# Optimization experiments

Measured on AMD Instinct MI355X. Metric: run time of the kernel, lower is better.

The kernel has to match this reference:

```python
import jax, jax.numpy as jnp
import numpy as np

V, EH, EO, H, O = 32000, 512, 256, 512, 256
S, B = 128, 32
THRESH = 1e-6


def _uniform(key, shape, fan_in):
    bound = 1.0 / np.sqrt(fan_in)
    return jax.random.uniform(key, shape, jnp.float32, -bound, bound)


def setup_inputs() -> dict:
    key = jax.random.key(0)
    ks = jax.random.split(key, 12)
    return {
        "input": jax.random.randint(ks[0], (S, B), 0, V, dtype=jnp.int32),
        # embedding_layer: Linear(V,EH), Linear(EH,EO); stored (in,out)
        "W1": _uniform(ks[1], (V, EH), V),
        "b1": _uniform(ks[2], (EH,), V),
        "W2": _uniform(ks[3], (EH, EO), EH),
        "b2": _uniform(ks[4], (EO,), EH),
        # GRU weights (PyTorch layout: gates stacked r,z,n)
        "W_ih": _uniform(ks[5], (3 * H, EO), H),
        "W_hh": _uniform(ks[6], (3 * H, H), H),
        "b_ih": _uniform(ks[7], (3 * H,), H),
        "b_hh": _uniform(ks[8], (3 * H,), H),
        # head: Linear(H,O)
        "W3": _uniform(ks[9], (H, O), H),
        "b3": _uniform(ks[10], (O,), H),
    }


def reference(input, W1, b1, W2, b2, W_ih, W_hh, b_ih, b_hh, W3, b3):
    thr = lambda x: jnp.where(x > THRESH, x, 0.0)  # nn.Threshold(1e-6, 0)
    # one_hot(input, V) @ W1 == row gather of W1 (same math, no O(V) GEMM)
    emb = thr(thr(W1[input] + b1) @ W2 + b2)  # (S, B, EO)

    # GRU: precompute input projections for all timesteps
    x_proj = emb @ W_ih.T + b_ih  # (S, B, 3H)
    h0 = jnp.zeros((B, H), jnp.float32)

    def step(h, xp):
        gh = h @ W_hh.T + b_hh
        xr, xz, xn = jnp.split(xp, 3, axis=-1)
        hr, hz, hn = jnp.split(gh, 3, axis=-1)
        r = jax.nn.sigmoid(xr + hr)
        z = jax.nn.sigmoid(xz + hz)
        n = jnp.tanh(xn + r * hn)
        h_new = (1.0 - z) * n + z * h
        return h_new, None

    hT, _ = jax.lax.scan(step, h0, x_proj)  # final hidden (B, H)
    # linear head on h_n (dropout in eval mode = identity); torch h_n is (1,B,H)
    out = hT[None, :, :] @ W3 + b3  # (1, B, O)
    return out
```

## Files before the change

### kernel.cpp

```cpp
#include <hip/hip_runtime.h>
#include <cstddef>

#define THRESH 1e-6f
#define SPIN_LIMIT (1 << 20)

__device__ __forceinline__ float thrf(float x) { return x > THRESH ? x : 0.0f; }
__device__ __forceinline__ float sigm(float x) { return 1.0f / (1.0f + expf(-x)); }
__device__ __forceinline__ void fma4(float4& c, float a, float4 b) {
    c.x += a * b.x; c.y += a * b.y; c.z += a * b.z; c.w += a * b.w;
}
__device__ __forceinline__ void macc4(float4& a, float4 w, float4 h) {
    a.x += w.x * h.x; a.y += w.y * h.y; a.z += w.z * h.z; a.w += w.w * h.w;
}
__device__ __forceinline__ float hsum4(float4 a) { return a.x + a.y + a.z + a.w; }

__global__ __launch_bounds__(256) void k_embed_gemm(const int* __restrict__ tok,
                                                    const float* __restrict__ W1,
                                                    const float* __restrict__ b1,
                                                    const float* __restrict__ W2,
                                                    const float* __restrict__ b2,
                                                    float* __restrict__ emb) {
    constexpr int BM = 64, BN = 64, BK = 32, K = 512, N = 256;
    __shared__ float As[BK][BM + 1];
    __shared__ float Bs[BK][BN];

    const int tid = threadIdx.x;
    const int bm = blockIdx.x * BM;
    const int bn = blockIdx.y * BN;
    const int tn = (tid & 15) * 4;
    const int tm = (tid >> 4) * 4;

    float acc[4][4] = {};

    for (int k0 = 0; k0 < K; k0 += BK) {
        for (int i = tid; i < BM * BK / 4; i += 256) {
            int c4 = (i & (BK / 4 - 1)) * 4;
            int r  = i / (BK / 4);
            int tv = tok[bm + r];
            float4 v  = *(const float4*)(W1 + (size_t)tv * K + k0 + c4);
            float4 bb = *(const float4*)(b1 + k0 + c4);
            As[c4 + 0][r] = thrf(v.x + bb.x);
            As[c4 + 1][r] = thrf(v.y + bb.y);
            As[c4 + 2][r] = thrf(v.z + bb.z);
            As[c4 + 3][r] = thrf(v.w + bb.w);
        }
        for (int i = tid; i < BK * BN / 4; i += 256) {
            int n4 = (i & 15) * 4;
            int kk = i >> 4;
            *(float4*)&Bs[kk][n4] = *(const float4*)(W2 + (size_t)(k0 + kk) * N + bn + n4);
        }
        __syncthreads();

        for (int k = 0; k < BK; ++k) {
            float a0 = As[k][tm + 0], a1 = As[k][tm + 1];
            float a2 = As[k][tm + 2], a3 = As[k][tm + 3];
            float b0 = Bs[k][tn + 0], b1v = Bs[k][tn + 1];
            float b2v = Bs[k][tn + 2], b3v = Bs[k][tn + 3];
            acc[0][0] += a0 * b0;  acc[0][1] += a0 * b1v;
            acc[0][2] += a0 * b2v; acc[0][3] += a0 * b3v;
            acc[1][0] += a1 * b0;  acc[1][1] += a1 * b1v;
            acc[1][2] += a1 * b2v; acc[1][3] += a1 * b3v;
            acc[2][0] += a2 * b0;  acc[2][1] += a2 * b1v;
            acc[2][2] += a2 * b2v; acc[2][3] += a2 * b3v;
            acc[3][0] += a3 * b0;  acc[3][1] += a3 * b1v;
            acc[3][2] += a3 * b2v; acc[3][3] += a3 * b3v;
        }
        __syncthreads();
    }

    const float4 bv = *(const float4*)(b2 + bn + tn);
    for (int i = 0; i < 4; ++i) {
        int m = bm + tm + i;
        float4 o;
        o.x = thrf(acc[i][0] + bv.x);
        o.y = thrf(acc[i][1] + bv.y);
        o.z = thrf(acc[i][2] + bv.z);
        o.w = thrf(acc[i][3] + bv.w);
        *(float4*)(emb + (size_t)m * N + bn + tn) = o;
    }
}

__global__ __launch_bounds__(256) void k_xproj(const float* __restrict__ emb,
                                               const float* __restrict__ W_ih,
                                               const float* __restrict__ b_ih,
                                               float* __restrict__ xp) {
    constexpr int BM = 128, BJ = 64, BK = 32, K = 256, J = 1536;
    __shared__ __align__(16) float As[BK][BM + 4];
    __shared__ __align__(16) float Bs[BK][BJ + 4];
    const int tid = threadIdx.x;
    const int bm = blockIdx.x * BM;
    const int bj = blockIdx.y * BJ;
    const int tj = (tid & 15) * 4;
    const int tm = (tid >> 4) * 8;

    float4 acc[8];
#pragma unroll
    for (int i = 0; i < 8; ++i) acc[i] = make_float4(0.f, 0.f, 0.f, 0.f);

    for (int k0 = 0; k0 < K; k0 += BK) {
#pragma unroll
        for (int p = 0; p < 4; ++p) {
            int i = tid + p * 256;
            int c4 = (i & 7) * 4, r = i >> 3;
            float4 v = *(const float4*)(emb + (size_t)(bm + r) * K + k0 + c4);
            As[c4 + 0][r] = v.x; As[c4 + 1][r] = v.y;
            As[c4 + 2][r] = v.z; As[c4 + 3][r] = v.w;
        }
#pragma unroll
        for (int p = 0; p < 2; ++p) {
            int i = tid + p * 256;
            int c4 = (i & 7) * 4, r = i >> 3;
            float4 v = *(const float4*)(W_ih + (size_t)(bj + r) * K + k0 + c4);
            Bs[c4 + 0][r] = v.x; Bs[c4 + 1][r] = v.y;
            Bs[c4 + 2][r] = v.z; Bs[c4 + 3][r] = v.w;
        }
        __syncthreads();

#pragma unroll 8
        for (int k = 0; k < BK; ++k) {
            float4 b4 = *(const float4*)&Bs[k][tj];
            float4 a0 = *(const float4*)&As[k][tm];
            float4 a1 = *(const float4*)&As[k][tm + 4];
            fma4(acc[0], a0.x, b4); fma4(acc[1], a0.y, b4);
            fma4(acc[2], a0.z, b4); fma4(acc[3], a0.w, b4);
            fma4(acc[4], a1.x, b4); fma4(acc[5], a1.y, b4);
            fma4(acc[6], a1.z, b4); fma4(acc[7], a1.w, b4);
        }
        __syncthreads();
    }

    const float4 bb = *(const float4*)(b_ih + bj + tj);
#pragma unroll
    for (int i = 0; i < 8; ++i) {
        float4 o = make_float4(acc[i].x + bb.x, acc[i].y + bb.y,
                               acc[i].z + bb.z, acc[i].w + bb.w);
        *(float4*)(xp + (size_t)(bm + tm + i) * J + bj + tj) = o;
    }
}

__global__ __launch_bounds__(256, 1) void k_scan(const float* __restrict__ xp,
                                                 const float* __restrict__ W_hh,
                                                 const float* __restrict__ b_hh,
                                                 unsigned long long* __restrict__ hx,
                                                 float* __restrict__ h_out) {
    constexpr int CH = 576;
    __shared__ __align__(16) float hl[2][4 * CH];
    const int tid  = threadIdx.x;
    const int g    = blockIdx.x & 7;
    const int m    = blockIdx.x >> 3;
    const int lane = tid & 63;
    const int wave = tid >> 6;
    const int kc   = lane & 15;
    const int jlow = lane >> 4;
    const int jglob = m * 16 + wave * 4 + jlow;
    const int hoff  = kc * 36;

    float4 wr[8], wz[8], wn[8];
#pragma unroll
    for (int i = 0; i < 8; ++i) {
        const int k = kc * 32 + i * 4;
        wr[i] = *(const float4*)(W_hh + (size_t)jglob * 512 + k);
        wz[i] = *(const float4*)(W_hh + (size_t)(512 + jglob) * 512 + k);
        wn[i] = *(const float4*)(W_hh + (size_t)(1024 + jglob) * 512 + k);
    }

    const int bg = g * 4 + kc;
    float bhr = 0.f, bhz = 0.f, bhn = 0.f, hprev = 0.f;
    if (kc < 4) {
        bhr = b_hh[jglob];
        bhz = b_hh[512 + jglob];
        bhn = b_hh[1024 + jglob];
    }

    for (int i = tid; i < 4 * CH; i += 256) hl[0][i] = 0.f;

    const int sflat = tid * 8;
    const int sb = sflat >> 9, sk = sflat & 511;
    const int sdst = sb * CH + sk + ((sk >> 5) << 2);

    for (int t = 0; t < 128; ++t) {
        float xr = 0.f, xz = 0.f, xn = 0.f;
        if (kc < 4) {
            const float* xrow = xp + (size_t)(t * 32 + bg) * 1536;
            xr = xrow[jglob];
            xz = xrow[512 + jglob];
            xn = xrow[1024 + jglob];
        }

        if (t > 0) {
            const unsigned tag = (unsigned)t;
            unsigned long long* base = hx + (size_t)(t & 1) * 16384
                                          + (size_t)(g * 4) * 512 + sflat;
            unsigned long long v[8];
#pragma unroll
            for (int p = 0; p < 8; ++p)
                v[p] = __hip_atomic_load(base + p, __ATOMIC_RELAXED, __HIP_MEMORY_SCOPE_AGENT);
            int spins = 0;
            for (;;) {
                bool all = true;
#pragma unroll
                for (int p = 0; p < 8; ++p) {
                    if ((unsigned)(v[p] >> 32) != tag) {
                        all = false;
                        v[p] = __hip_atomic_load(base + p, __ATOMIC_RELAXED, __HIP_MEMORY_SCOPE_AGENT);
                    }
                }
                if (all || ++spins > SPIN_LIMIT) break;
                __builtin_amdgcn_s_sleep(1);
            }
            union { unsigned u; float f; } c0, c1, c2, c3, c4, c5, c6, c7;
            c0.u = (unsigned)v[0]; c1.u = (unsigned)v[1];
            c2.u = (unsigned)v[2]; c3.u = (unsigned)v[3];
            c4.u = (unsigned)v[4]; c5.u = (unsigned)v[5];
            c6.u = (unsigned)v[6]; c7.u = (unsigned)v[7];
            *(float4*)&hl[t & 1][sdst]     = make_float4(c0.f, c1.f, c2.f, c3.f);
            *(float4*)&hl[t & 1][sdst + 4] = make_float4(c4.f, c5.f, c6.f, c7.f);
        }
        __syncthreads();

        const float* hb = hl[t & 1];
        float p[3][4];
#pragma unroll
        for (int b = 0; b < 4; ++b) {
            float4 ar = make_float4(0.f, 0.f, 0.f, 0.f), az = ar, an = ar;
            const float* h0 = hb + b * CH + hoff;
#pragma unroll
            for (int i = 0; i < 8; ++i) {
                float4 h4 = *(const float4*)(h0 + i * 4);
                macc4(ar, wr[i], h4);
                macc4(az, wz[i], h4);
                macc4(an, wn[i], h4);
            }
            p[0][b] = hsum4(ar); p[1][b] = hsum4(az); p[2][b] = hsum4(an);
        }

#pragma unroll
        for (int gg = 0; gg < 3; ++gg)
#pragma unroll
            for (int b = 0; b < 4; ++b) {
                float v = p[gg][b];
                v += __shfl_xor(v, 1);
                v += __shfl_xor(v, 2);
                v += __shfl_xor(v, 4);
                v += __shfl_xor(v, 8);
                p[gg][b] = v;
            }

        if (kc < 4) {
            float sr, sz, sn;
            if      (kc == 0) { sr = p[0][0]; sz = p[1][0]; sn = p[2][0]; }
            else if (kc == 1) { sr = p[0][1]; sz = p[1][1]; sn = p[2][1]; }
            else if (kc == 2) { sr = p[0][2]; sz = p[1][2]; sn = p[2][2]; }
            else              { sr = p[0][3]; sz = p[1][3]; sn = p[2][3]; }
            float r  = sigm(xr + sr + bhr);
            float z  = sigm(xz + sz + bhz);
            float n  = tanhf(xn + r * (sn + bhn));
            float hn = (1.0f - z) * n + z * hprev;
            hprev = hn;
            if (t < 127) {
                union { float f; unsigned u; } cv; cv.f = hn;
                __hip_atomic_store(hx + (size_t)((t + 1) & 1) * 16384
                                      + (size_t)bg * 512 + jglob,
                                   ((unsigned long long)(unsigned)(t + 1) << 32) | cv.u,
                                   __ATOMIC_RELAXED, __HIP_MEMORY_SCOPE_AGENT);
            } else {
                h_out[(size_t)bg * 512 + jglob] = hn;
            }
        }
    }
}

__global__ __launch_bounds__(256) void k_head(const float* __restrict__ h,
                                              const float* __restrict__ W3,
                                              const float* __restrict__ b3,
                                              float* __restrict__ out) {
    const int b = blockIdx.x;
    const int o = threadIdx.x;
    const float* hrow = h + (size_t)b * 512;
    float acc = b3[o];
#pragma unroll 8
    for (int k = 0; k < 512; ++k)
        acc += hrow[k] * W3[(size_t)k * 256 + o];
    out[(size_t)b * 256 + o] = acc;
}

extern "C" void kernel_launch(void* const* d_in, const int* in_sizes, int n_in,
                              void* d_out, int out_size, void* d_ws, size_t ws_size,
                              hipStream_t stream) {
    const int*   tok  = (const int*)d_in[0];
    const float* W1   = (const float*)d_in[1];
    const float* b1   = (const float*)d_in[2];
    const float* W2   = (const float*)d_in[3];
    const float* b2   = (const float*)d_in[4];
    const float* W_ih = (const float*)d_in[5];
    const float* W_hh = (const float*)d_in[6];
    const float* b_ih = (const float*)d_in[7];
    const float* b_hh = (const float*)d_in[8];
    const float* W3   = (const float*)d_in[9];
    const float* b3   = (const float*)d_in[10];
    float* out = (float*)d_out;
    (void)ws_size;

    float* ws   = (float*)d_ws;
    float* emb  = ws;
    float* xp   = ws + 1048576;
    unsigned long long* hx = (unsigned long long*)(ws + 7340032);
    float* hfin = ws + 7340032 + 65536;

    {
        dim3 grd(4096 / 64, 256 / 64);
        k_embed_gemm<<<grd, 256, 0, stream>>>(tok, W1, b1, W2, b2, emb);
    }
    {
        dim3 grd(4096 / 128, 1536 / 64);
        k_xproj<<<grd, 256, 0, stream>>>(emb, W_ih, b_ih, xp);
    }
    k_scan<<<256, 256, 0, stream>>>(xp, W_hh, b_hh, hx, hfin);

    k_head<<<32, 256, 0, stream>>>(hfin, W3, b3, out);
}
```

Before: 873.7 us.

## Stage W_hh slice in swizzled LDS instead of per-thread registers in GRU scan

The recurrent weight slice for each block (3 gates x 16 rows x 512) moves out of 96 per-thread float registers into a 96KB shared-memory buffer with an XOR swizzle on float4 index to avoid bank conflicts. The inner loop now reads weights from LDS each timestep, reusing each weight load across 4 batch columns. The aim is lower register pressure and possibly fewer spills, at the cost of extra LDS traffic on the latency-critical sequential scan path. The launch-bounds minimum-blocks hint is also removed.

```diff
diff --git a/kernel.cpp b/kernel.cpp
--- a/kernel.cpp
+++ b/kernel.cpp
@@ -138,13 +138,15 @@
     }
 }
 
-__global__ __launch_bounds__(256, 1) void k_scan(const float* __restrict__ xp,
-                                                 const float* __restrict__ W_hh,
-                                                 const float* __restrict__ b_hh,
-                                                 unsigned long long* __restrict__ hx,
-                                                 float* __restrict__ h_out) {
+__global__ __launch_bounds__(256) void k_scan(const float* __restrict__ xp,
+                                              const float* __restrict__ W_hh,
+                                              const float* __restrict__ b_hh,
+                                              unsigned long long* __restrict__ hx,
+                                              float* __restrict__ h_out) {
     constexpr int CH = 576;
+    __shared__ __align__(16) float Wl[3 * 16 * 512];
     __shared__ __align__(16) float hl[2][4 * CH];
+
     const int tid  = threadIdx.x;
     const int g    = blockIdx.x & 7;
     const int m    = blockIdx.x >> 3;
@@ -152,17 +154,25 @@
     const int wave = tid >> 6;
     const int kc   = lane & 15;
     const int jlow = lane >> 4;
-    const int jglob = m * 16 + wave * 4 + jlow;
+    const int wjj  = wave * 4 + jlow;
+    const int jglob = m * 16 + wjj;
     const int hoff  = kc * 36;
-
-    float4 wr[8], wz[8], wn[8];
-#pragma unroll
-    for (int i = 0; i < 8; ++i) {
-        const int k = kc * 32 + i * 4;
-        wr[i] = *(const float4*)(W_hh + (size_t)jglob * 512 + k);
-        wz[i] = *(const float4*)(W_hh + (size_t)(512 + jglob) * 512 + k);
-        wn[i] = *(const float4*)(W_hh + (size_t)(1024 + jglob) * 512 + k);
-    }
+    const int kx    = kc & 7;
+
+    for (int idx = tid; idx < 3 * 16 * 128; idx += 256) {
+        const int gg  = idx >> 11;
+        const int rem = idx & 2047;
+        const int jj  = rem >> 7;
+        const int f4  = rem & 127;
+        const int kcs = f4 >> 3, ii = f4 & 7;
+        const int f4s = (kcs << 3) | (ii ^ (kcs & 7));
+        const float4 v = *(const float4*)(W_hh + (size_t)(gg * 512 + m * 16 + jj) * 512 + f4 * 4);
+        *(float4*)&Wl[(((gg << 4) + jj) << 9) + f4s * 4] = v;
+    }
+
+    const float* w0 = &Wl[(( 0 + wjj) << 9) + kc * 32];
+    const float* w1 = &Wl[((16 + wjj) << 9) + kc * 32];
+    const float* w2 = &Wl[((32 + wjj) << 9) + kc * 32];
 
     const int bg = g * 4 + kc;
     float bhr = 0.f, bhz = 0.f, bhn = 0.f, hprev = 0.f;
@@ -219,19 +229,30 @@
         __syncthreads();
 
         const float* hb = hl[t & 1];
+        float4 ar[4], az[4], an[4];
+#pragma unroll
+        for (int b = 0; b < 4; ++b) {
+            ar[b] = make_float4(0.f, 0.f, 0.f, 0.f);
+            az[b] = ar[b]; an[b] = ar[b];
+        }
+#pragma unroll
+        for (int i = 0; i < 8; ++i) {
+            const int io = (i ^ kx) << 2;
+            const float4 wrv = *(const float4*)(w0 + io);
+            const float4 wzv = *(const float4*)(w1 + io);
+            const float4 wnv = *(const float4*)(w2 + io);
+#pragma unroll
+            for (int b = 0; b < 4; ++b) {
+                const float4 h4 = *(const float4*)(hb + b * CH + hoff + i * 4);
+                macc4(ar[b], wrv, h4);
+                macc4(az[b], wzv, h4);
+                macc4(an[b], wnv, h4);
+            }
+        }
         float p[3][4];
 #pragma unroll
         for (int b = 0; b < 4; ++b) {
-            float4 ar = make_float4(0.f, 0.f, 0.f, 0.f), az = ar, an = ar;
-            const float* h0 = hb + b * CH + hoff;
-#pragma unroll
-            for (int i = 0; i < 8; ++i) {
-                float4 h4 = *(const float4*)(h0 + i * 4);
-                macc4(ar, wr[i], h4);
-                macc4(az, wz[i], h4);
-                macc4(an, wn[i], h4);
-            }
-            p[0][b] = hsum4(ar); p[1][b] = hsum4(az); p[2][b] = hsum4(an);
+            p[0][b] = hsum4(ar[b]); p[1][b] = hsum4(az[b]); p[2][b] = hsum4(an[b]);
         }
 
 #pragma unroll
```

Result: slower. 901.3 us (+3.2%).
